# Kernel tuning notes

Hardware: AMD Instinct MI355X
Metric: run time of the kernel (lower is better)

## Reference

```python
import jax, jax.numpy as jnp
import numpy as np
from jax.scipy.special import erf

B, S, D = 8, 512, 512
H = 8            # num_heads per half
DH = D // 2      # 256, per-branch model dim
DFF = 2048
HOUT = 2


def _layernorm(x, g, b, eps=1e-6):
    mu = jnp.mean(x, axis=-1, keepdims=True)
    var = jnp.mean(jnp.square(x - mu), axis=-1, keepdims=True)
    return (x - mu) / jnp.sqrt(var + eps) * g + b


def _rescale_dist(w):
    one = jnp.float32(1.0)
    return (one + jnp.exp(one)) / (one + jnp.exp(one - w))


def _mha(xin, wq, bq, wk, bk, wv, bv, wo, bo, maskf, adjoin, dist):
    b, s, dm = xin.shape
    dep = dm // H
    def heads(t):
        return t.reshape(b, s, H, dep).transpose(0, 2, 1, 3)  # (b,h,s,dep)
    q = heads(xin @ wq + bq)
    k = heads(xin @ wk + bk)
    v = heads(xin @ wv + bv)
    scores = jnp.einsum('bhqd,bhkd->bhqk', q, k)
    scale = jnp.sqrt(jnp.float32(dep))
    if dist is not None:
        scores = jax.nn.relu(scores) * _rescale_dist(dist) / scale
    else:
        scores = scores / scale
    scores = scores + maskf * jnp.float32(-1e9)
    if adjoin is not None:
        scores = scores + adjoin
    attn = jax.nn.softmax(scores, axis=-1)
    out = jnp.einsum('bhqk,bhkd->bhqd', attn, v).transpose(0, 2, 1, 3).reshape(b, s, dm)
    return out @ wo + bo, attn


def setup_inputs() -> dict:
    key = jax.random.key(0)
    ks = jax.random.split(key, 32)
    init = lambda k, shp: (jax.random.normal(k, shp, dtype=jnp.float32) * 0.02)
    inp = {
        'x': jax.random.normal(ks[0], (B, S, D), dtype=jnp.float32),
        'adjoin_matrix': jax.random.normal(ks[1], (B, 1, S, S), dtype=jnp.float32),
        'dist_matrix': jax.random.uniform(ks[2], (B, 1, S, S), dtype=jnp.float32),
        # mha1 (adjoin branch)
        'wq1': init(ks[3], (DH, DH)), 'bq1': jnp.zeros((DH,), jnp.float32),
        'wk1': init(ks[4], (DH, DH)), 'bk1': jnp.zeros((DH,), jnp.float32),
        'wv1': init(ks[5], (DH, DH)), 'bv1': jnp.zeros((DH,), jnp.float32),
        'wo1': init(ks[6], (DH, DH)), 'bo1': jnp.zeros((DH,), jnp.float32),
        # mha2 (distance branch)
        'wq2': init(ks[7], (DH, DH)), 'bq2': jnp.zeros((DH,), jnp.float32),
        'wk2': init(ks[8], (DH, DH)), 'bk2': jnp.zeros((DH,), jnp.float32),
        'wv2': init(ks[9], (DH, DH)), 'bv2': jnp.zeros((DH,), jnp.float32),
        'wo2': init(ks[10], (DH, DH)), 'bo2': jnp.zeros((DH,), jnp.float32),
        # BANLayer
        'vnet_w': init(ks[11], (DH, 2 * DH)), 'vnet_b': jnp.zeros((2 * DH,), jnp.float32),
        'qnet_w': init(ks[12], (DH, 2 * DH)), 'qnet_b': jnp.zeros((2 * DH,), jnp.float32),
        'h_mat': init(ks[13], (1, HOUT, 1, 2 * DH)),
        'h_bias': init(ks[14], (1, HOUT, 1, 1)),
        'bn_gamma': jnp.ones((D,), jnp.float32), 'bn_beta': jnp.zeros((D,), jnp.float32),
        'bn_mean': jnp.zeros((D,), jnp.float32), 'bn_var': jnp.ones((D,), jnp.float32),
        # LayerNorms
        'ln1_g': jnp.ones((D,), jnp.float32), 'ln1_b': jnp.zeros((D,), jnp.float32),
        'ln2_g': jnp.ones((D,), jnp.float32), 'ln2_b': jnp.zeros((D,), jnp.float32),
        # FFN
        'ffn_w1': init(ks[15], (D, DFF)), 'ffn_b1': jnp.zeros((DFF,), jnp.float32),
        'ffn_w2': init(ks[16], (DFF, D)), 'ffn_b2': jnp.zeros((D,), jnp.float32),
        # padding mask (int -> cast), 1 = masked
        'encoder_padding_mask': jax.random.randint(ks[17], (B, 1, 1, S), 0, 2, dtype=jnp.int32),
    }
    return inp


def reference(x, adjoin_matrix, dist_matrix,
              wq1, bq1, wk1, bk1, wv1, bv1, wo1, bo1,
              wq2, bq2, wk2, bk2, wv2, bv2, wo2, bo2,
              vnet_w, vnet_b, qnet_w, qnet_b, h_mat, h_bias,
              bn_gamma, bn_beta, bn_mean, bn_var,
              ln1_g, ln1_b, ln2_g, ln2_b,
              ffn_w1, ffn_b1, ffn_w2, ffn_b2,
              encoder_padding_mask):
    maskf = encoder_padding_mask.astype(jnp.float32)
    x1, x2 = jnp.split(x, 2, axis=-1)
    # local branch: adjoin bias, no distance
    x_l, aw_local = _mha(x1, wq1, bq1, wk1, bk1, wv1, bv1, wo1, bo1, maskf, adjoin_matrix, None)
    # global branch: relu + distance rescale, no adjoin
    x_g, aw_global = _mha(x2, wq2, bq2, wk2, bk2, wv2, bv2, wo2, bo2, maskf, None, dist_matrix)
    # BANLayer (h_out=2 <= c, eval mode; p_net is identity for rows=1)
    v_ = jax.nn.relu(x_l @ vnet_w + vnet_b)   # (B,S,2*DH)
    q_ = jax.nn.relu(x_g @ qnet_w + qnet_b)
    att_maps = jnp.einsum('xhyk,bvk,bqk->bhvq', h_mat, v_, q_) + h_bias  # (B,HOUT,S,S)
    logits = jnp.einsum('bvk,bhvq,bqk->bvk', v_, att_maps, q_)           # sum over h
    logits = (logits - bn_mean) / jnp.sqrt(bn_var + 1e-3) * bn_gamma + bn_beta
    attn_output = logits * jnp.concatenate([x_l, x_g], axis=-1)
    out1 = _layernorm(x + attn_output, ln1_g, ln1_b)
    h = out1 @ ffn_w1 + ffn_b1
    h = 0.5 * h * (1.0 + erf(h / jnp.sqrt(jnp.float32(2.0))))  # exact gelu
    ffn_out = h @ ffn_w2 + ffn_b2
    out2 = _layernorm(out1 + ffn_out, ln2_g, ln2_b)
    return (out2, aw_local, aw_global)
```

## Files before the change

### kernel.cpp

```cpp
#include <hip/hip_runtime.h>
#include <hip/hip_bf16.h>

typedef __hip_bfloat16 bf16;
typedef __attribute__((ext_vector_type(8))) short bf16x8;
typedef __attribute__((ext_vector_type(4))) float f32x4;
typedef __attribute__((ext_vector_type(4))) _Float16 f16x4;

#define BB 8
#define SS 512
#define DD 512
#define NH 8
#define DHm 256
#define DFF 2048

__device__ __forceinline__ void gl_lds16(const void* g, void* l) {
  __builtin_amdgcn_global_load_lds((const __attribute__((address_space(1))) void*)g,
                                   (__attribute__((address_space(3))) void*)l, 16, 0, 0);
}

__device__ __forceinline__ bf16x8 cvt8(const float* p) {
  union { bf16x8 v; bf16 h[8]; } u;
  float4 f0 = *(const float4*)p, f1 = *(const float4*)(p + 4);
  u.h[0]=__float2bfloat16(f0.x); u.h[1]=__float2bfloat16(f0.y);
  u.h[2]=__float2bfloat16(f0.z); u.h[3]=__float2bfloat16(f0.w);
  u.h[4]=__float2bfloat16(f1.x); u.h[5]=__float2bfloat16(f1.y);
  u.h[6]=__float2bfloat16(f1.z); u.h[7]=__float2bfloat16(f1.w);
  return u.v;
}

template<int BM, int BN, int SMODE, int BIASM, int ACT, int VTM>
__global__ __launch_bounds__(256)
void gemm2(const bf16* __restrict__ A, const bf16* __restrict__ B,
           const float* __restrict__ bias, float* __restrict__ Cf,
           bf16* __restrict__ Cb, int K, int lda, int ldb, int ldc,
           long long sA, long long sB, long long sC, int sBias,
           bf16* __restrict__ Cb2, const float* __restrict__ cscale)
{
  __shared__ bf16 As[BM * 32];
  __shared__ bf16 Bs[BN * 32];
  const int t = threadIdx.x, lane = t & 63, wave = t >> 6;
  const int l15 = lane & 15, quad = lane >> 4;
  constexpr int WMT = BM / 32, WNT = BN / 32;
  const int wm = (wave & 1) * (BM / 2), wn = (wave >> 1) * (BN / 2);
  const int row0 = blockIdx.y * BM, col0 = blockIdx.x * BN;
  const bf16* Ab = A + (long long)blockIdx.z * sA + (long long)row0 * lda;
  const bf16* Bb = B + (long long)blockIdx.z * sB + (long long)col0 * ldb;
  const int srow = wave * 16 + (lane >> 2), skc = (lane & 3) << 3;

  f32x4 acc[WMT][WNT] = {};

  for (int k0 = 0; k0 < K; k0 += 32) {
#pragma unroll
    for (int j = 0; j < BM / 64; j++)
      gl_lds16(Ab + (long long)(srow + j * 64) * lda + k0 + skc,
               (char*)As + wave * 1024 + j * 4096);
#pragma unroll
    for (int j = 0; j < BN / 64; j++)
      gl_lds16(Bb + (long long)(srow + j * 64) * ldb + k0 + skc,
               (char*)Bs + wave * 1024 + j * 4096);
    __syncthreads();
    bf16x8 af[WMT], bfr[WNT];
#pragma unroll
    for (int i = 0; i < WMT; i++) af[i]  = *(const bf16x8*)&As[(wm + i * 16 + l15) * 32 + quad * 8];
#pragma unroll
    for (int j = 0; j < WNT; j++) bfr[j] = *(const bf16x8*)&Bs[(wn + j * 16 + l15) * 32 + quad * 8];
#pragma unroll
    for (int i = 0; i < WMT; i++)
#pragma unroll
      for (int j = 0; j < WNT; j++)
        acc[i][j] = __builtin_amdgcn_mfma_f32_16x16x32_bf16(af[i], bfr[j], acc[i][j], 0, 0, 0);
    __syncthreads();
  }

  float sb = 0.f;
  if (BIASM == 2) sb = bias[0] + bias[1];
#pragma unroll
  for (int i = 0; i < WMT; i++)
#pragma unroll
    for (int j = 0; j < WNT; j++) {
      int col = col0 + wn + j * 16 + l15;
      float bv = (BIASM == 1) ? bias[(long long)blockIdx.z * sBias + col] : sb;
      float vv[4];
#pragma unroll
      for (int r = 0; r < 4; r++) {
        float v = acc[i][j][r] + bv;
        if (ACT == 1) v = fmaxf(v, 0.f);
        if (ACT == 2) v = 0.5f * v * (1.f + erff(v * 0.70710678118654752f));
        vv[r] = v;
      }
      const int rowb = row0 + wm + i * 16 + (quad << 2);
      if (VTM == 1 && col >= 512) {
        int hh = (col - 512) >> 5, dep = (col - 512) & 31;
        int bidx = rowb >> 9, kpos = rowb & 511;
        long long vo = ((((long long)blockIdx.z * 8 + bidx) * 8 + hh) * 64 + (kpos >> 3)) * 32 + dep;
        bf16 h0 = __float2bfloat16(vv[0]), h1 = __float2bfloat16(vv[1]);
        bf16 h2 = __float2bfloat16(vv[2]), h3 = __float2bfloat16(vv[3]);
        short4 pk;
        pk.x = *(short*)&h0; pk.y = *(short*)&h1; pk.z = *(short*)&h2; pk.w = *(short*)&h3;
        *(short4*)(Cb2 + vo * 8 + (kpos & 7)) = pk;
      } else {
#pragma unroll
        for (int r = 0; r < 4; r++) {
          long long ci = (long long)blockIdx.z * sC + (long long)(rowb + r) * ldc + col;
          if (SMODE & 1) Cf[ci] = vv[r];
          if (SMODE & 2) Cb[ci] = __float2bfloat16(vv[r]);
          if (VTM == 2) Cb2[ci] = __float2bfloat16(vv[r] * cscale[col]);
        }
      }
    }
}

__global__ __launch_bounds__(256)
void eprep(const float* __restrict__ adjoin, const float* __restrict__ dist,
           const int* __restrict__ mask, _Float16* __restrict__ EP)
{
  const int qt = blockIdx.x, kt = blockIdx.y, zz = blockIdx.z;
  const int b = zz & 7, branch = zz >> 3;
  const float* E = (branch ? dist : adjoin) + ((long long)b * SS + qt * 64) * SS + kt * 128;
  __shared__ float tile[64][129];
  const int t = threadIdx.x;
  const int r0 = t >> 2, c0 = (t & 3) * 32;
#pragma unroll
  for (int jj = 0; jj < 8; jj++) {
    float4 f = *(const float4*)(E + (long long)r0 * SS + c0 + jj * 4);
    tile[r0][c0 + jj * 4 + 0] = f.x; tile[r0][c0 + jj * 4 + 1] = f.y;
    tile[r0][c0 + jj * 4 + 2] = f.z; tile[r0][c0 + jj * 4 + 3] = f.w;
  }
  __syncthreads();
  const int lane = t & 63, wq = t >> 6, l15 = lane & 15, quad = lane >> 4;
  const float scale_inv = 0.17677669529663688f;
  f16x4* out = (f16x4*)EP;
#pragma unroll
  for (int kcl = 0; kcl < 8; kcl++) {
    int kk = kcl * 16 + l15;
    f16x4 o;
    if (branch == 0) {
      float mv = (float)mask[b * SS + kt * 128 + kk] * -1e9f;
#pragma unroll
      for (int r = 0; r < 4; r++)
        o[r] = (_Float16)(tile[wq * 16 + quad * 4 + r][kk] + mv);
    } else {
#pragma unroll
      for (int r = 0; r < 4; r++) {
        float ev = tile[wq * 16 + quad * 4 + r][kk];
        o[r] = (_Float16)(3.7182818284590452f / (1.f + __expf(1.f - ev)) * scale_inv);
      }
    }
    out[((((long long)zz * 8 + qt) * 4 + wq) * 32 + (kt * 8 + kcl)) * 64 + lane] = o;
  }
}

__global__ __launch_bounds__(256, 3)
void attn_fused(const bf16* __restrict__ QKV1, const bf16* __restrict__ QKV2,
                const bf16* __restrict__ VT, const int* __restrict__ mask,
                const _Float16* __restrict__ EP,
                float* __restrict__ awl, float* __restrict__ awg,
                bf16* __restrict__ ctx1, bf16* __restrict__ ctx2)
{
  const int qt = blockIdx.x, h = blockIdx.y, zz = blockIdx.z;
  const int b = zz & 7, branch = zz >> 3;
  const bf16* __restrict__ QKV = branch ? QKV2 : QKV1;
  float* __restrict__ aw = branch ? awg : awl;
  bf16* __restrict__ ctx = branch ? ctx2 : ctx1;

  const int t = threadIdx.x, lane = t & 63, wave = t >> 6;
  const int l15 = lane & 15, quad = lane >> 4;
  __shared__ bf16x8 Vt[64][32];
  alignas(16) __shared__ bf16 Pl[4][2048];
  __shared__ float mvalf[512];

  const bf16* VTs = VT + ((long long)zz * 8 + h) * 16384;
#pragma unroll
  for (int j = 0; j < 8; j++)
    gl_lds16(VTs + (long long)t * 8 + j * 2048, (char*)Vt + wave * 1024 + j * 4096);

  { int2 m2 = *(const int2*)(mask + b * SS + t * 2);
    mvalf[t * 2]     = (float)m2.x * -1e9f;
    mvalf[t * 2 + 1] = (float)m2.y * -1e9f; }

  const int q0 = qt * 64 + wave * 16;
  const bf16* Qb = QKV + ((long long)(b * SS + q0)) * 768 + h * 32;
  bf16x8 qfrag = *(const bf16x8*)(Qb + (long long)l15 * 768 + quad * 8);
  __syncthreads();

  const float scale_inv = 0.17677669529663688f;
  const bf16* Kb = QKV + (long long)b * SS * 768 + 256 + h * 32;
  const f16x4* Ep = (const f16x4*)EP + (((long long)zz * 8 + qt) * 4 + wave) * 2048;

  float rsum[4] = {0.f, 0.f, 0.f, 0.f};
#pragma unroll
  for (int kc = 0; kc < 32; kc++) {
    const int kpos = kc * 16 + l15;
    bf16x8 kfrag = *(const bf16x8*)(Kb + (long long)kpos * 768 + quad * 8);
    f16x4 e4 = Ep[kc * 64 + lane];
    f32x4 a = __builtin_amdgcn_mfma_f32_16x16x32_bf16(qfrag, kfrag, f32x4{0.f,0.f,0.f,0.f}, 0, 0, 0);
    float mv = (branch == 0) ? 0.f : mvalf[kpos];
#pragma unroll
    for (int r = 0; r < 4; r++) {
      float s = (branch == 0) ? fmaf(a[r], scale_inv, (float)e4[r])
                              : fmaf(fmaxf(a[r], 0.f), (float)e4[r], mv);
      rsum[r] += __expf(s);
    }
  }
  float rsi[4];
#pragma unroll
  for (int r = 0; r < 4; r++) {
    float v = rsum[r];
    v += __shfl_xor(v, 1, 16);
    v += __shfl_xor(v, 2, 16);
    v += __shfl_xor(v, 4, 16);
    v += __shfl_xor(v, 8, 16);
    rsi[r] = 1.f / v;
  }

  f32x4 oacc[2] = {};
  bf16* Pw = Pl[wave];
  const int rkey = ((l15 >> 2) ^ l15) & 3;
  float* awp = aw + (((long long)(b * NH + h) * SS + q0)) * SS;

#pragma unroll
  for (int c = 0; c < 4; c++) {
#pragma unroll
    for (int kcl = 0; kcl < 8; kcl++) {
      const int kc = c * 8 + kcl;
      const int kpos = kc * 16 + l15;
      bf16x8 kfrag = *(const bf16x8*)(Kb + (long long)kpos * 768 + quad * 8);
      f16x4 e4 = Ep[kc * 64 + lane];
      f32x4 a = __builtin_amdgcn_mfma_f32_16x16x32_bf16(qfrag, kfrag, f32x4{0.f,0.f,0.f,0.f}, 0, 0, 0);
      float mv = (branch == 0) ? 0.f : mvalf[kpos];
#pragma unroll
      for (int r = 0; r < 4; r++) {
        float s = (branch == 0) ? fmaf(a[r], scale_inv, (float)e4[r])
                                : fmaf(fmaxf(a[r], 0.f), (float)e4[r], mv);
        float p = __expf(s) * rsi[r];
        awp[(long long)(quad * 4 + r) * SS + kpos] = p;
        const int key = (quad ^ r) & 3;
        const int off = (quad * 4 + r) * 256 + (((kcl * 16 + l15) * 2) ^ (key << 5));
        *(bf16*)((char*)Pw + off) = __float2bfloat16(p);
      }
    }
    __builtin_amdgcn_s_setprio(1);
#pragma unroll
    for (int k2 = 0; k2 < 4; k2++) {
      const int off = l15 * 256 + ((k2 * 64 + quad * 16) ^ (rkey << 5));
      bf16x8 afr = *(const bf16x8*)((const char*)Pw + off);
      const int blk = (c * 4 + k2) * 4 + quad;
      oacc[0] = __builtin_amdgcn_mfma_f32_16x16x32_bf16(afr, Vt[blk][l15],      oacc[0], 0, 0, 0);
      oacc[1] = __builtin_amdgcn_mfma_f32_16x16x32_bf16(afr, Vt[blk][16 + l15], oacc[1], 0, 0, 0);
    }
    __builtin_amdgcn_s_setprio(0);
  }

#pragma unroll
  for (int n = 0; n < 2; n++)
#pragma unroll
    for (int r = 0; r < 4; r++) {
      int q = q0 + quad * 4 + r;
      ctx[(long long)(b * SS + q) * DHm + h * 32 + n * 16 + l15] =
          __float2bfloat16(oacc[n][r]);
    }
}

__device__ __forceinline__ void tr_tile(const float* __restrict__ src, bf16* __restrict__ dst,
                                        int K, int N, int tile) {
  __shared__ float tl[32][33];
  int tilesN = N >> 5;
  int tk = tile / tilesN, tn = tile % tilesN;
  int c = threadIdx.x & 31, r0 = threadIdx.x >> 5;
#pragma unroll
  for (int i = 0; i < 4; i++) {
    int r = r0 + i * 8;
    tl[r][c] = src[(long long)(tk * 32 + r) * N + tn * 32 + c];
  }
  __syncthreads();
#pragma unroll
  for (int i = 0; i < 4; i++) {
    int r = r0 + i * 8;
    dst[(long long)(tn * 32 + r) * K + tk * 32 + c] = __float2bfloat16(tl[c][r]);
  }
}

__global__ __launch_bounds__(256)
void pack_all(const float* wq1, const float* wk1, const float* wv1,
              const float* wq2, const float* wk2, const float* wv2,
              const float* wo1, const float* wo2,
              const float* vnet_w, const float* qnet_w,
              const float* ffn_w1, const float* ffn_w2,
              const float* bq1, const float* bk1, const float* bv1,
              const float* bq2, const float* bk2, const float* bv2,
              const float* bo1, const float* bo2,
              const float* vnet_b, const float* qnet_b,
              const float* h_mat,
              const float* x,
              bf16* WB1, bf16* WB2, bf16* woT1, bf16* woT2,
              bf16* vnetT, bf16* qnetT, bf16* f1T, bf16* f2T,
              float* BB1v, float* BB2v, float* BOv, float* VQb, float* HSv, bf16* xb)
{
  int blk = blockIdx.x;
  if (blk < 64)        { tr_tile(wq1, WB1,            256, 256, blk); return; }
  if (blk < 128)       { tr_tile(wk1, WB1 + 256*256,  256, 256, blk-64); return; }
  if (blk < 192)       { tr_tile(wv1, WB1 + 512*256,  256, 256, blk-128); return; }
  if (blk < 256)       { tr_tile(wq2, WB2,            256, 256, blk-192); return; }
  if (blk < 320)       { tr_tile(wk2, WB2 + 256*256,  256, 256, blk-256); return; }
  if (blk < 384)       { tr_tile(wv2, WB2 + 512*256,  256, 256, blk-320); return; }
  if (blk < 448)       { tr_tile(wo1, woT1,           256, 256, blk-384); return; }
  if (blk < 512)       { tr_tile(wo2, woT2,           256, 256, blk-448); return; }
  if (blk < 640)       { tr_tile(vnet_w, vnetT,       256, 512, blk-512); return; }
  if (blk < 768)       { tr_tile(qnet_w, qnetT,       256, 512, blk-640); return; }
  if (blk < 1792)      { tr_tile(ffn_w1, f1T,         512, 2048, blk-768); return; }
  if (blk < 2816)      { tr_tile(ffn_w2, f2T,         2048, 512, blk-1792); return; }
  if (blk < 3840) {
    long long i0 = (long long)(blk - 2816) * 2048 + threadIdx.x * 8;
    *(bf16x8*)(xb + i0) = cvt8(x + i0);
    return;
  }
  if (blk < 3846) {
    int b = blk - 3840;
    const float* src = b==0?bq1 : b==1?bk1 : b==2?bv1 : b==3?bq2 : b==4?bk2 : bv2;
    float* dst = (b < 3 ? BB1v : BB2v) + (b % 3) * 256;
    dst[threadIdx.x] = src[threadIdx.x];
    return;
  }
  if (blk < 3848) {
    int b = blk - 3846;
    BOv[b * 256 + threadIdx.x] = (b ? bo2 : bo1)[threadIdx.x];
    return;
  }
  if (blk < 3852) {
    int b = blk - 3848;
    const float* src = (b < 2) ? vnet_b : qnet_b;
    VQb[b * 256 + threadIdx.x] = src[(b & 1) * 256 + threadIdx.x];
    return;
  }
  {
    int t = threadIdx.x;
    HSv[t]       = h_mat[t]       + h_mat[512 + t];
    HSv[t + 256] = h_mat[256 + t] + h_mat[768 + t];
  }
}

__global__ __launch_bounds__(256)
void tr_qn(const bf16* __restrict__ Qn, bf16* __restrict__ QnT)
{
  int b = blockIdx.z, tk = blockIdx.y, tn = blockIdx.x;
  __shared__ bf16 tl[32][33];
  int c = threadIdx.x & 31, r0 = threadIdx.x >> 5;
  const bf16* src = Qn + (long long)b * 512 * 512;
  bf16* dst = QnT + (long long)b * 512 * 512;
#pragma unroll
  for (int i = 0; i < 4; i++) { int r = r0 + i * 8; tl[r][c] = src[(tk * 32 + r) * 512 + tn * 32 + c]; }
  __syncthreads();
#pragma unroll
  for (int i = 0; i < 4; i++) { int r = r0 + i * 8; dst[(tn * 32 + r) * 512 + tk * 32 + c] = tl[c][r]; }
}

__global__ __launch_bounds__(256)
void bn_gate_ln1_kernel(const float* __restrict__ x, const bf16* __restrict__ vbuf,
                        const float* __restrict__ T, const float* __restrict__ xl,
                        const float* __restrict__ xg,
                        const float* __restrict__ bng, const float* __restrict__ bnb,
                        const float* __restrict__ bnm, const float* __restrict__ bnv,
                        const float* __restrict__ lng, const float* __restrict__ lnb,
                        float* __restrict__ out1, bf16* __restrict__ out1b)
{
  const int row = blockIdx.x;
  const int t = threadIdx.x;
  const int lane = t & 63, wave = t >> 6;
  __shared__ float red[8];
  float val[2];
#pragma unroll
  for (int i = 0; i < 2; i++) {
    int c = t + i * 256;
    long long idx = (long long)row * DD + c;
    float lg = __bfloat162float(vbuf[idx]) * T[idx];
    float bn = (lg - bnm[c]) / sqrtf(bnv[c] + 1e-3f) * bng[c] + bnb[c];
    float gate = (c < DHm) ? xl[(long long)row * DHm + c] : xg[(long long)row * DHm + (c - DHm)];
    val[i] = x[idx] + bn * gate;
  }
  float s = val[0] + val[1];
#pragma unroll
  for (int o = 32; o > 0; o >>= 1) s += __shfl_xor(s, o);
  if (lane == 0) red[wave] = s;
  __syncthreads();
  float mu = (red[0] + red[1] + red[2] + red[3]) * (1.f / 512.f);
  float d0 = val[0] - mu, d1 = val[1] - mu;
  float vs = d0 * d0 + d1 * d1;
#pragma unroll
  for (int o = 32; o > 0; o >>= 1) vs += __shfl_xor(vs, o);
  if (lane == 0) red[4 + wave] = vs;
  __syncthreads();
  float inv = 1.f / sqrtf((red[4] + red[5] + red[6] + red[7]) * (1.f / 512.f) + 1e-6f);
  float o0 = d0 * inv * lng[t] + lnb[t];
  float o1 = d1 * inv * lng[t + 256] + lnb[t + 256];
  out1[(long long)row * DD + t] = o0;
  out1[(long long)row * DD + t + 256] = o1;
  out1b[(long long)row * DD + t] = __float2bfloat16(o0);
  out1b[(long long)row * DD + t + 256] = __float2bfloat16(o1);
}

__global__ __launch_bounds__(256)
void ln2_kernel(const float* __restrict__ a, const float* __restrict__ b2,
                const float* __restrict__ g, const float* __restrict__ bta,
                float* __restrict__ out)
{
  const int row = blockIdx.x;
  const int t = threadIdx.x;
  const int lane = t & 63, wave = t >> 6;
  __shared__ float red[8];
  float v0 = a[(long long)row * DD + t]       + b2[(long long)row * DD + t];
  float v1 = a[(long long)row * DD + t + 256] + b2[(long long)row * DD + t + 256];
  float s = v0 + v1;
#pragma unroll
  for (int o = 32; o > 0; o >>= 1) s += __shfl_xor(s, o);
  if (lane == 0) red[wave] = s;
  __syncthreads();
  float mu = (red[0] + red[1] + red[2] + red[3]) * (1.f / 512.f);
  float d0 = v0 - mu, d1 = v1 - mu;
  float vs = d0 * d0 + d1 * d1;
#pragma unroll
  for (int o = 32; o > 0; o >>= 1) vs += __shfl_xor(vs, o);
  if (lane == 0) red[4 + wave] = vs;
  __syncthreads();
  float inv = 1.f / sqrtf((red[4] + red[5] + red[6] + red[7]) * (1.f / 512.f) + 1e-6f);
  out[(long long)row * DD + t]       = d0 * inv * g[t]       + bta[t];
  out[(long long)row * DD + t + 256] = d1 * inv * g[t + 256] + bta[t + 256];
}

extern "C" void kernel_launch(void* const* d_in, const int* in_sizes, int n_in,
                              void* d_out, int out_size, void* d_ws, size_t ws_size,
                              hipStream_t stream) {
  const float* x      = (const float*)d_in[0];
  const float* adjoin = (const float*)d_in[1];
  const float* dist   = (const float*)d_in[2];
  const float* wq1=(const float*)d_in[3],  *bq1=(const float*)d_in[4];
  const float* wk1=(const float*)d_in[5],  *bk1=(const float*)d_in[6];
  const float* wv1=(const float*)d_in[7],  *bv1=(const float*)d_in[8];
  const float* wo1=(const float*)d_in[9],  *bo1=(const float*)d_in[10];
  const float* wq2=(const float*)d_in[11], *bq2=(const float*)d_in[12];
  const float* wk2=(const float*)d_in[13], *bk2=(const float*)d_in[14];
  const float* wv2=(const float*)d_in[15], *bv2=(const float*)d_in[16];
  const float* wo2=(const float*)d_in[17], *bo2=(const float*)d_in[18];
  const float* vnet_w=(const float*)d_in[19], *vnet_b=(const float*)d_in[20];
  const float* qnet_w=(const float*)d_in[21], *qnet_b=(const float*)d_in[22];
  const float* h_mat=(const float*)d_in[23], *h_bias=(const float*)d_in[24];
  const float* bn_g=(const float*)d_in[25], *bn_b=(const float*)d_in[26];
  const float* bn_m=(const float*)d_in[27], *bn_v=(const float*)d_in[28];
  const float* ln1_g=(const float*)d_in[29], *ln1_b=(const float*)d_in[30];
  const float* ln2_g=(const float*)d_in[31], *ln2_b=(const float*)d_in[32];
  const float* ffn_w1=(const float*)d_in[33], *ffn_b1=(const float*)d_in[34];
  const float* ffn_w2=(const float*)d_in[35], *ffn_b2=(const float*)d_in[36];
  const int* mask = (const int*)d_in[37];

  char* base = (char*)d_ws;
  size_t off = 0;
  auto alloc = [&](size_t bytes) { char* p = base + off; off += (bytes + 255) & ~(size_t)255; return p; };
  bf16*  xb    = (bf16*) alloc(4096LL*512*2);
  bf16*  WB1   = (bf16*) alloc(768*256*2);
  bf16*  WB2   = (bf16*) alloc(768*256*2);
  float* BB1v  = (float*)alloc(768*4);
  float* BB2v  = (float*)alloc(768*4);
  float* BOv   = (float*)alloc(512*4);
  float* VQb   = (float*)alloc(1024*4);
  float* HSv   = (float*)alloc(512*4);
  bf16*  woT1  = (bf16*) alloc(256*256*2);
  bf16*  woT2  = (bf16*) alloc(256*256*2);
  bf16*  vnetT = (bf16*) alloc(512*256*2);
  bf16*  qnetT = (bf16*) alloc(512*256*2);
  bf16*  f1T   = (bf16*) alloc(2048*512*2);
  bf16*  f2T   = (bf16*) alloc(512*2048*2);
  bf16*  QKV1  = (bf16*) alloc(4096LL*768*2);
  bf16*  QKV2  = (bf16*) alloc(4096LL*768*2);
  bf16*  VTb   = (bf16*) alloc(2LL*8*8*512*32*2);
  _Float16* EP = (_Float16*)alloc(8388608);
  bf16*  CTX   = (bf16*) alloc(4096LL*256*2);
  bf16*  CTX2  = (bf16*) alloc(4096LL*256*2);
  float* XL    = (float*)alloc(4096LL*256*4);
  float* XG    = (float*)alloc(4096LL*256*4);
  bf16*  XLb   = (bf16*) alloc(4096LL*256*2);
  bf16*  XGb   = (bf16*) alloc(4096LL*256*2);
  bf16*  Vn    = (bf16*) alloc(4096LL*512*2);
  bf16*  Qn    = (bf16*) alloc(4096LL*512*2);
  bf16*  QnT   = (bf16*) alloc(4096LL*512*2);
  bf16*  VH    = (bf16*) alloc(4096LL*512*2);
  bf16*  G     = (bf16*) alloc(8LL*512*512*2);
  float* T     = (float*)alloc(4096LL*512*4);
  float* OUT1  = (float*)alloc(4096LL*512*4);
  bf16*  OUT1b = (bf16*) alloc(4096LL*512*2);
  bf16*  H     = (bf16*) alloc(4096LL*2048*2);
  float* FFNO  = (float*)alloc(4096LL*512*4);

  float* out2 = (float*)d_out;
  float* awl  = out2 + 2097152LL;
  float* awg  = awl + 16777216LL;

  const int MR = BB * SS;
  const long long GST = (long long)SS * SS;

  pack_all<<<dim3(3853), 256, 0, stream>>>(
      wq1, wk1, wv1, wq2, wk2, wv2, wo1, wo2, vnet_w, qnet_w, ffn_w1, ffn_w2,
      bq1, bk1, bv1, bq2, bk2, bv2, bo1, bo2, vnet_b, qnet_b, h_mat, x,
      WB1, WB2, woT1, woT2, vnetT, qnetT, f1T, f2T, BB1v, BB2v, BOv, VQb, HSv, xb);

  eprep<<<dim3(8, 4, 16), 256, 0, stream>>>(adjoin, dist, mask, EP);

  gemm2<128,128,2,1,0,1><<<dim3(6, 32, 2), 256, 0, stream>>>(
      xb, WB1, BB1v, nullptr, QKV1, 256, 512, 256, 768,
      256LL, 768LL*256, 4096LL*768, 768, VTb, nullptr);

  attn_fused<<<dim3(8, NH, 16), 256, 0, stream>>>(
      QKV1, QKV2, VTb, mask, EP, awl, awg, CTX, CTX2);

  gemm2<64,64,3,1,0,0><<<dim3(4, 64, 2), 256, 0, stream>>>(
      CTX, woT1, BOv, XL, XLb, 256, 256, 256, 256,
      4096LL*256, 256LL*256, 4096LL*256, 256, nullptr, nullptr);

  gemm2<64,64,2,1,1,2><<<dim3(8, 64, 2), 256, 0, stream>>>(
      XLb, vnetT, VQb, nullptr, Vn, 256, 256, 256, 512,
      4096LL*256, 512LL*256, 4096LL*512, 512, VH, HSv);

  tr_qn<<<dim3(16, 16, BB), 256, 0, stream>>>(Qn, QnT);
  gemm2<64,64,2,2,0,0><<<dim3(8, 8, BB), 256, 0, stream>>>(
      VH, Qn, h_bias, nullptr, G, 512, 512, 512, 512, GST, GST, GST, 0, nullptr, nullptr);
  gemm2<64,64,1,0,0,0><<<dim3(8, 8, BB), 256, 0, stream>>>(
      G, QnT, nullptr, T, nullptr, 512, 512, 512, 512, GST, GST, GST, 0, nullptr, nullptr);

  bn_gate_ln1_kernel<<<dim3(MR), 256, 0, stream>>>(
      x, Vn, T, XL, XG, bn_g, bn_b, bn_m, bn_v, ln1_g, ln1_b, OUT1, OUT1b);

  gemm2<128,128,2,1,2,0><<<dim3(16, 32, 1), 256, 0, stream>>>(
      OUT1b, f1T, ffn_b1, nullptr, H, 512, 512, 512, 2048, 0, 0, 0, 0, nullptr, nullptr);
  gemm2<64,128,1,1,0,0><<<dim3(4, 64, 1), 256, 0, stream>>>(
      H, f2T, ffn_b2, FFNO, nullptr, 2048, 2048, 2048, 512, 0, 0, 0, 0, nullptr, nullptr);

  ln2_kernel<<<dim3(MR), 256, 0, stream>>>(OUT1, FFNO, ln2_g, ln2_b, out2);
}
```

Before: 502.1 us.

## Single-pass attention softmax, head-major Q/K layout, coalesced eprep loads, larger GEMM tiles

Attention now computes scores and exponentials once. Unnormalized probabilities are kept as packed bf16 in registers and used for P·V, and the context and attention-weight outputs are normalized at the end, which removes the separate row-sum pass. The QKV GEMM writes Q and K in a per-head contiguous layout, so K loads in the attention kernel read contiguous 64-byte rows instead of rows strided by 768 elements. eprep reads tiles with coalesced row-wise float4 loads, and several downstream GEMMs switch to larger tiles. The tradeoff is lower occupancy from the 64-register stash, and the stored attention weights are rounded to bf16 precision.

```diff
diff --git a/kernel.cpp b/kernel.cpp
--- a/kernel.cpp
+++ b/kernel.cpp
@@ -5,6 +5,7 @@
 typedef __attribute__((ext_vector_type(8))) short bf16x8;
 typedef __attribute__((ext_vector_type(4))) float f32x4;
 typedef __attribute__((ext_vector_type(4))) _Float16 f16x4;
+typedef unsigned int u32;
 
 #define BB 8
 #define SS 512
@@ -89,15 +90,23 @@
         vv[r] = v;
       }
       const int rowb = row0 + wm + i * 16 + (quad << 2);
-      if (VTM == 1 && col >= 512) {
-        int hh = (col - 512) >> 5, dep = (col - 512) & 31;
-        int bidx = rowb >> 9, kpos = rowb & 511;
-        long long vo = ((((long long)blockIdx.z * 8 + bidx) * 8 + hh) * 64 + (kpos >> 3)) * 32 + dep;
-        bf16 h0 = __float2bfloat16(vv[0]), h1 = __float2bfloat16(vv[1]);
-        bf16 h2 = __float2bfloat16(vv[2]), h3 = __float2bfloat16(vv[3]);
-        short4 pk;
-        pk.x = *(short*)&h0; pk.y = *(short*)&h1; pk.z = *(short*)&h2; pk.w = *(short*)&h3;
-        *(short4*)(Cb2 + vo * 8 + (kpos & 7)) = pk;
+      if (VTM == 1) {
+        const int bidx = rowb >> 9, kpos = rowb & 511;
+        const long long zz8 = (long long)blockIdx.z * 8 + bidx;
+        if (col < 512) {
+          const int part = col >> 8, hh = (col >> 5) & 7, dep = col & 31;
+          bf16* dst = Cb2 + (((zz8 * 8 + hh) * 2 + part) * 512 + (long long)kpos) * 32 + dep;
+#pragma unroll
+          for (int r = 0; r < 4; r++) dst[r * 32] = __float2bfloat16(vv[r]);
+        } else {
+          const int hh = (col - 512) >> 5, dep = (col - 512) & 31;
+          long long vo = ((zz8 * 8 + hh) * 64 + (kpos >> 3)) * 32 + dep;
+          bf16 h0 = __float2bfloat16(vv[0]), h1 = __float2bfloat16(vv[1]);
+          bf16 h2 = __float2bfloat16(vv[2]), h3 = __float2bfloat16(vv[3]);
+          short4 pk;
+          pk.x = *(short*)&h0; pk.y = *(short*)&h1; pk.z = *(short*)&h2; pk.w = *(short*)&h3;
+          *(short4*)(Cb + vo * 8 + (kpos & 7)) = pk;
+        }
       } else {
 #pragma unroll
         for (int r = 0; r < 4; r++) {
@@ -119,12 +128,13 @@
   const float* E = (branch ? dist : adjoin) + ((long long)b * SS + qt * 64) * SS + kt * 128;
   __shared__ float tile[64][129];
   const int t = threadIdx.x;
-  const int r0 = t >> 2, c0 = (t & 3) * 32;
+  const int r0 = t >> 5, c4 = (t & 31) * 4;
 #pragma unroll
   for (int jj = 0; jj < 8; jj++) {
-    float4 f = *(const float4*)(E + (long long)r0 * SS + c0 + jj * 4);
-    tile[r0][c0 + jj * 4 + 0] = f.x; tile[r0][c0 + jj * 4 + 1] = f.y;
-    tile[r0][c0 + jj * 4 + 2] = f.z; tile[r0][c0 + jj * 4 + 3] = f.w;
+    int row = r0 + jj * 8;
+    float4 f = *(const float4*)(E + (long long)row * SS + c4);
+    tile[row][c4 + 0] = f.x; tile[row][c4 + 1] = f.y;
+    tile[row][c4 + 2] = f.z; tile[row][c4 + 3] = f.w;
   }
   __syncthreads();
   const int lane = t & 63, wq = t >> 6, l15 = lane & 15, quad = lane >> 4;
@@ -150,16 +160,14 @@
   }
 }
 
-__global__ __launch_bounds__(256, 3)
-void attn_fused(const bf16* __restrict__ QKV1, const bf16* __restrict__ QKV2,
-                const bf16* __restrict__ VT, const int* __restrict__ mask,
-                const _Float16* __restrict__ EP,
+__global__ __launch_bounds__(256, 2)
+void attn_fused(const bf16* __restrict__ QKF, const bf16* __restrict__ VT,
+                const int* __restrict__ mask, const _Float16* __restrict__ EP,
                 float* __restrict__ awl, float* __restrict__ awg,
                 bf16* __restrict__ ctx1, bf16* __restrict__ ctx2)
 {
   const int qt = blockIdx.x, h = blockIdx.y, zz = blockIdx.z;
   const int b = zz & 7, branch = zz >> 3;
-  const bf16* __restrict__ QKV = branch ? QKV2 : QKV1;
   float* __restrict__ aw = branch ? awg : awl;
   bf16* __restrict__ ctx = branch ? ctx2 : ctx1;
 
@@ -179,44 +187,19 @@
     mvalf[t * 2 + 1] = (float)m2.y * -1e9f; }
 
   const int q0 = qt * 64 + wave * 16;
-  const bf16* Qb = QKV + ((long long)(b * SS + q0)) * 768 + h * 32;
-  bf16x8 qfrag = *(const bf16x8*)(Qb + (long long)l15 * 768 + quad * 8);
+  const bf16* Qbase = QKF + ((long long)zz * 8 + h) * 2 * 16384;
+  const bf16* Kbase = Qbase + 16384;
+  bf16x8 qfrag = *(const bf16x8*)(Qbase + (long long)(q0 + l15) * 32 + quad * 8);
   __syncthreads();
 
   const float scale_inv = 0.17677669529663688f;
-  const bf16* Kb = QKV + (long long)b * SS * 768 + 256 + h * 32;
   const f16x4* Ep = (const f16x4*)EP + (((long long)zz * 8 + qt) * 4 + wave) * 2048;
 
+  u32 eh[64];
   float rsum[4] = {0.f, 0.f, 0.f, 0.f};
-#pragma unroll
-  for (int kc = 0; kc < 32; kc++) {
-    const int kpos = kc * 16 + l15;
-    bf16x8 kfrag = *(const bf16x8*)(Kb + (long long)kpos * 768 + quad * 8);
-    f16x4 e4 = Ep[kc * 64 + lane];
-    f32x4 a = __builtin_amdgcn_mfma_f32_16x16x32_bf16(qfrag, kfrag, f32x4{0.f,0.f,0.f,0.f}, 0, 0, 0);
-    float mv = (branch == 0) ? 0.f : mvalf[kpos];
-#pragma unroll
-    for (int r = 0; r < 4; r++) {
-      float s = (branch == 0) ? fmaf(a[r], scale_inv, (float)e4[r])
-                              : fmaf(fmaxf(a[r], 0.f), (float)e4[r], mv);
-      rsum[r] += __expf(s);
-    }
-  }
-  float rsi[4];
-#pragma unroll
-  for (int r = 0; r < 4; r++) {
-    float v = rsum[r];
-    v += __shfl_xor(v, 1, 16);
-    v += __shfl_xor(v, 2, 16);
-    v += __shfl_xor(v, 4, 16);
-    v += __shfl_xor(v, 8, 16);
-    rsi[r] = 1.f / v;
-  }
-
   f32x4 oacc[2] = {};
-  bf16* Pw = Pl[wave];
+  short* Pw = (short*)Pl[wave];
   const int rkey = ((l15 >> 2) ^ l15) & 3;
-  float* awp = aw + (((long long)(b * NH + h) * SS + q0)) * SS;
 
 #pragma unroll
   for (int c = 0; c < 4; c++) {
@@ -224,20 +207,29 @@
     for (int kcl = 0; kcl < 8; kcl++) {
       const int kc = c * 8 + kcl;
       const int kpos = kc * 16 + l15;
-      bf16x8 kfrag = *(const bf16x8*)(Kb + (long long)kpos * 768 + quad * 8);
+      bf16x8 kfrag = *(const bf16x8*)(Kbase + (long long)kpos * 32 + quad * 8);
       f16x4 e4 = Ep[kc * 64 + lane];
       f32x4 a = __builtin_amdgcn_mfma_f32_16x16x32_bf16(qfrag, kfrag, f32x4{0.f,0.f,0.f,0.f}, 0, 0, 0);
       float mv = (branch == 0) ? 0.f : mvalf[kpos];
+      u32 p01 = 0, p23 = 0;
 #pragma unroll
       for (int r = 0; r < 4; r++) {
         float s = (branch == 0) ? fmaf(a[r], scale_inv, (float)e4[r])
                                 : fmaf(fmaxf(a[r], 0.f), (float)e4[r], mv);
-        float p = __expf(s) * rsi[r];
-        awp[(long long)(quad * 4 + r) * SS + kpos] = p;
+        float e = __expf(s);
+        rsum[r] += e;
+        u32 xb = __float_as_uint(e);
+        u32 b16 = (xb + 0x7FFFu + ((xb >> 16) & 1u)) >> 16;
+        if (r == 0)      p01 = b16;
+        else if (r == 1) p01 |= b16 << 16;
+        else if (r == 2) p23 = b16;
+        else             p23 |= b16 << 16;
         const int key = (quad ^ r) & 3;
         const int off = (quad * 4 + r) * 256 + (((kcl * 16 + l15) * 2) ^ (key << 5));
-        *(bf16*)((char*)Pw + off) = __float2bfloat16(p);
+        *(short*)((char*)Pw + off) = (short)b16;
       }
+      eh[kc * 2]     = p01;
+      eh[kc * 2 + 1] = p23;
     }
     __builtin_amdgcn_s_setprio(1);
 #pragma unroll
@@ -251,14 +243,38 @@
     __builtin_amdgcn_s_setprio(0);
   }
 
+  float rsi[4];
+#pragma unroll
+  for (int r = 0; r < 4; r++) {
+    float v = rsum[r];
+    v += __shfl_xor(v, 1, 16);
+    v += __shfl_xor(v, 2, 16);
+    v += __shfl_xor(v, 4, 16);
+    v += __shfl_xor(v, 8, 16);
+    rsi[r] = 1.f / v;
+  }
+
 #pragma unroll
   for (int n = 0; n < 2; n++)
 #pragma unroll
     for (int r = 0; r < 4; r++) {
       int q = q0 + quad * 4 + r;
       ctx[(long long)(b * SS + q) * DHm + h * 32 + n * 16 + l15] =
-          __float2bfloat16(oacc[n][r]);
+          __float2bfloat16(oacc[n][r] * rsi[r]);
     }
+
+  float* awp = aw + (((long long)(b * NH + h) * SS + q0)) * SS;
+#pragma unroll
+  for (int kc = 0; kc < 32; kc++) {
+    u32 p01 = eh[kc * 2], p23 = eh[kc * 2 + 1];
+#pragma unroll
+    for (int r = 0; r < 4; r++) {
+      u32 bits = (r == 0) ? (p01 & 0xFFFFu) : (r == 1) ? (p01 >> 16)
+               : (r == 2) ? (p23 & 0xFFFFu) : (p23 >> 16);
+      float e = __uint_as_float(bits << 16);
+      awp[(long long)(quad * 4 + r) * SS + kc * 16 + l15] = e * rsi[r];
+    }
+  }
 }
 
 __device__ __forceinline__ void tr_tile(const float* __restrict__ src, bf16* __restrict__ dst,
@@ -468,8 +484,7 @@
   bf16*  qnetT = (bf16*) alloc(512*256*2);
   bf16*  f1T   = (bf16*) alloc(2048*512*2);
   bf16*  f2T   = (bf16*) alloc(512*2048*2);
-  bf16*  QKV1  = (bf16*) alloc(4096LL*768*2);
-  bf16*  QKV2  = (bf16*) alloc(4096LL*768*2);
+  bf16*  QKF   = (bf16*) alloc(16LL*8*2*512*32*2);
   bf16*  VTb   = (bf16*) alloc(2LL*8*8*512*32*2);
   _Float16* EP = (_Float16*)alloc(8388608);
   bf16*  CTX   = (bf16*) alloc(4096LL*256*2);
@@ -503,25 +518,25 @@
 
   eprep<<<dim3(8, 4, 16), 256, 0, stream>>>(adjoin, dist, mask, EP);
 
-  gemm2<128,128,2,1,0,1><<<dim3(6, 32, 2), 256, 0, stream>>>(
-      xb, WB1, BB1v, nullptr, QKV1, 256, 512, 256, 768,
-      256LL, 768LL*256, 4096LL*768, 768, VTb, nullptr);
+  gemm2<128,128,0,1,0,1><<<dim3(6, 32, 2), 256, 0, stream>>>(
+      xb, WB1, BB1v, nullptr, VTb, 256, 512, 256, 768,
+      256LL, 768LL*256, 0LL, 768, QKF, nullptr);
 
   attn_fused<<<dim3(8, NH, 16), 256, 0, stream>>>(
-      QKV1, QKV2, VTb, mask, EP, awl, awg, CTX, CTX2);
-
-  gemm2<64,64,3,1,0,0><<<dim3(4, 64, 2), 256, 0, stream>>>(
+      QKF, VTb, mask, EP, awl, awg, CTX, CTX2);
+
+  gemm2<64,128,3,1,0,0><<<dim3(2, 64, 2), 256, 0, stream>>>(
       CTX, woT1, BOv, XL, XLb, 256, 256, 256, 256,
       4096LL*256, 256LL*256, 4096LL*256, 256, nullptr, nullptr);
 
-  gemm2<64,64,2,1,1,2><<<dim3(8, 64, 2), 256, 0, stream>>>(
+  gemm2<128,128,2,1,1,2><<<dim3(4, 32, 2), 256, 0, stream>>>(
       XLb, vnetT, VQb, nullptr, Vn, 256, 256, 256, 512,
       4096LL*256, 512LL*256, 4096LL*512, 512, VH, HSv);
 
   tr_qn<<<dim3(16, 16, BB), 256, 0, stream>>>(Qn, QnT);
-  gemm2<64,64,2,2,0,0><<<dim3(8, 8, BB), 256, 0, stream>>>(
+  gemm2<64,128,2,2,0,0><<<dim3(4, 8, BB), 256, 0, stream>>>(
       VH, Qn, h_bias, nullptr, G, 512, 512, 512, 512, GST, GST, GST, 0, nullptr, nullptr);
-  gemm2<64,64,1,0,0,0><<<dim3(8, 8, BB), 256, 0, stream>>>(
+  gemm2<64,128,1,0,0,0><<<dim3(4, 8, BB), 256, 0, stream>>>(
       G, QnT, nullptr, T, nullptr, 512, 512, 512, 512, GST, GST, GST, 0, nullptr, nullptr);
 
   bn_gate_ln1_kernel<<<dim3(MR), 256, 0, stream>>>(
```

After: 463.9 us. 1.08x faster.
